# Kernel tuning notes

Measured on AMD Instinct MI355X. Metric: run time of the kernel, lower is better.

Reference implementation:

```python
import jax, jax.numpy as jnp
import numpy as np

B = 8192
D = 1024
NUM_HEADS = 16
HEAD_DIM = D // NUM_HEADS  # 64; only used as the softmax scale


def setup_inputs() -> dict:
    key = jax.random.key(0)
    ks = jax.random.split(key, 7)
    s = 1.0 / np.sqrt(D)
    return {
        "x": jax.random.normal(ks[0], (B, D), dtype=jnp.float32),
        "Wq": jax.random.normal(ks[1], (D, D), dtype=jnp.float32) * s,
        "bq": jax.random.normal(ks[2], (D,), dtype=jnp.float32) * s,
        "Wk": jax.random.normal(ks[3], (D, D), dtype=jnp.float32) * s,
        "bk": jax.random.normal(ks[4], (D,), dtype=jnp.float32) * s,
        "Wv": jax.random.normal(ks[5], (D, D), dtype=jnp.float32) * s,
        "bv": jax.random.normal(ks[6], (D,), dtype=jnp.float32) * s,
    }


def reference(x, Wq, bq, Wk, bk, Wv, bv):
    # Faithful to the torch module: x is 2D [B, D]; attention is over the batch axis.
    # nn.Linear computes x @ W.T + b
    Q = x @ Wq.T + bq            # [B, D]
    K = x @ Wk.T + bk            # [B, D]
    V = x @ Wv.T + bv            # [B, D]
    scale = 1.0 / jnp.sqrt(jnp.float32(HEAD_DIM))
    energy = (Q @ K.T) * scale   # [B, B]
    attn = jax.nn.softmax(energy, axis=-1)
    out = attn @ V               # [B, D]
    # torch: x.permute(0,1).contiguous().view(B, seq_len, -1) -> [B, D, 1]
    return out.reshape(B, D, 1)
```

## Files before the change

kernel.cpp:

```cpp
#include <hip/hip_runtime.h>
#include <hip/hip_bf16.h>

typedef _Float16 half_t;
typedef _Float16 f16x8 __attribute__((ext_vector_type(8)));
typedef _Float16 f16x4 __attribute__((ext_vector_type(4)));
typedef float f32x4 __attribute__((ext_vector_type(4)));
typedef float f32x16 __attribute__((ext_vector_type(16)));

#define B_ROWS 8192
#define D_DIM  1024

__device__ __forceinline__ void gload_lds16(const void* g, void* l)
{
    __builtin_amdgcn_global_load_lds((const __attribute__((address_space(1))) void*)g,
                                     (__attribute__((address_space(3))) void*)l, 16, 0, 0);
}

__global__ __launch_bounds__(256)
void cvt_f32_f16(const float* __restrict__ in, half_t* __restrict__ out, int n)
{
    int i = (blockIdx.x * 256 + threadIdx.x) * 4;
    int stride = gridDim.x * 256 * 4;
    for (; i < n; i += stride) {
        float4 v = *(const float4*)&in[i];
        f16x4 o;
        o[0] = (half_t)v.x; o[1] = (half_t)v.y; o[2] = (half_t)v.z; o[3] = (half_t)v.w;
        *(f16x4*)&out[i] = o;
    }
}

__global__ __launch_bounds__(256)
void transpose_h(const half_t* __restrict__ in, half_t* __restrict__ out, int R, int C)
{
    __shared__ half_t t[64][65];
    int tilesC = C >> 6;
    int bc = blockIdx.x % tilesC;
    int br = blockIdx.x / tilesC;
    int r0 = br * 64, c0 = bc * 64;
    for (int e = threadIdx.x; e < 64 * 64; e += 256) {
        int r = e >> 6, c = e & 63;
        t[r][c] = in[(size_t)(r0 + r) * C + (c0 + c)];
    }
    __syncthreads();
    for (int e = threadIdx.x; e < 64 * 64; e += 256) {
        int r = e >> 6, c = e & 63;
        out[(size_t)(c0 + r) * R + (r0 + c)] = t[c][r];
    }
}

template<int EPI>
__device__ __forceinline__ void gemm8_core(
    const half_t* __restrict__ A, const half_t* __restrict__ Bm,
    const float* __restrict__ aux, float* __restrict__ aux2, int zcol,
    void* __restrict__ Out,
    int lda, int ldb, int ldc, float scale,
    int row0, int col0, int ktile0, int nkt)
{
    __shared__ __align__(16) half_t smem[8 * 8192];
    half_t* As = smem;
    half_t* Bs = smem + 4 * 8192;

    const int tid  = threadIdx.x;
    const int lane = tid & 63;
    const int wid  = tid >> 6;
    const int wr   = wid >> 2;
    const int wcn  = wid & 3;
    const int l31  = lane & 31;
    const int l32  = lane >> 5;

    const int trow  = tid >> 3;
    const int tslot = (tid & 7) ^ (trow & 7);
    const char* Apan[2] = { (const char*)(A + (size_t)row0 * lda),
                            (const char*)(A + (size_t)(row0 + 128) * lda) };
    const char* Bpan[2] = { (const char*)(Bm + (size_t)col0 * ldb),
                            (const char*)(Bm + (size_t)(col0 + 128) * ldb) };
    const size_t aoff[2] = { (size_t)trow * lda * 2 + (size_t)tslot * 16,
                             (size_t)(trow + 64) * lda * 2 + (size_t)tslot * 16 };
    const size_t boff[2] = { (size_t)trow * ldb * 2 + (size_t)tslot * 16,
                             (size_t)(trow + 64) * ldb * 2 + (size_t)tslot * 16 };
    const int dstb[2] = { tid * 16, 8192 + tid * 16 };

    auto stageA = [&](int h, int s, int buf) {
        char* d = (char*)(As + (buf * 2 + h) * 8192);
        const char* g = Apan[h] + (size_t)(ktile0 + s) * 128;
        gload_lds16(g + aoff[0], d + dstb[0]);
        gload_lds16(g + aoff[1], d + dstb[1]);
    };
    auto stageB = [&](int h, int s, int buf) {
        char* d = (char*)(Bs + (buf * 2 + h) * 8192);
        const char* g = Bpan[h] + (size_t)(ktile0 + s) * 128;
        gload_lds16(g + boff[0], d + dstb[0]);
        gload_lds16(g + boff[1], d + dstb[1]);
    };
    auto rdA = [&](int mm, int kc, const half_t* base) -> f16x8 {
        int rih  = wr * 64 + mm * 32 + l31;
        int byte = rih * 128 + (((kc * 2 + l32) ^ (rih & 7)) << 4);
        return *(const f16x8*)((const char*)base + byte);
    };
    auto rdB = [&](int kc, const half_t* base) -> f16x8 {
        int rih  = wcn * 32 + l31;
        int byte = rih * 128 + (((kc * 2 + l32) ^ (rih & 7)) << 4);
        return *(const f16x8*)((const char*)base + byte);
    };

    f32x16 acc[2][2][2] = {};
    f16x8 af[2][4];
    f16x8 bfP[4], bfQ[4];

    {
        int s1 = (nkt > 1) ? 1 : 0;
        stageA(0, 0, 0); stageB(0, 0, 0); stageA(1, 0, 0); stageB(1, 0, 0);
        stageA(0, s1, 1); stageB(0, s1, 1);
    }
    asm volatile("s_waitcnt vmcnt(4)" ::: "memory");
    asm volatile("s_barrier" ::: "memory");

    for (int t = 0; t < nkt; ++t) {
        const int buf = t & 1;
        const half_t* A0 = As + (buf * 2 + 0) * 8192;
        const half_t* A1 = As + (buf * 2 + 1) * 8192;
        const half_t* B0 = Bs + (buf * 2 + 0) * 8192;
        const half_t* B1 = Bs + (buf * 2 + 1) * 8192;
        int t1  = t + 1; int t1s = (t1 < nkt) ? t1 : nkt - 1; int b1 = t1 & 1;
        int t2  = t + 2; int t2s = (t2 < nkt) ? t2 : nkt - 1;

        #pragma unroll
        for (int mm = 0; mm < 2; ++mm)
            #pragma unroll
            for (int kc = 0; kc < 4; ++kc) af[mm][kc] = rdA(mm, kc, A0);
        #pragma unroll
        for (int kc = 0; kc < 4; ++kc) bfP[kc] = rdB(kc, B0);
        stageA(1, t1s, b1);
        asm volatile("s_barrier" ::: "memory");
        __builtin_amdgcn_s_setprio(1);
        #pragma unroll
        for (int kc = 0; kc < 4; ++kc)
            #pragma unroll
            for (int mm = 0; mm < 2; ++mm)
                acc[0][mm][0] = __builtin_amdgcn_mfma_f32_32x32x16_f16(af[mm][kc], bfP[kc], acc[0][mm][0], 0, 0, 0);
        __builtin_amdgcn_s_setprio(0);
        asm volatile("s_barrier" ::: "memory");

        #pragma unroll
        for (int kc = 0; kc < 4; ++kc) bfQ[kc] = rdB(kc, B1);
        stageB(1, t1s, b1);
        asm volatile("s_barrier" ::: "memory");
        __builtin_amdgcn_s_setprio(1);
        #pragma unroll
        for (int kc = 0; kc < 4; ++kc)
            #pragma unroll
            for (int mm = 0; mm < 2; ++mm)
                acc[0][mm][1] = __builtin_amdgcn_mfma_f32_32x32x16_f16(af[mm][kc], bfQ[kc], acc[0][mm][1], 0, 0, 0);
        __builtin_amdgcn_s_setprio(0);
        asm volatile("s_barrier" ::: "memory");

        #pragma unroll
        for (int mm = 0; mm < 2; ++mm)
            #pragma unroll
            for (int kc = 0; kc < 4; ++kc) af[mm][kc] = rdA(mm, kc, A1);
        stageA(0, t2s, buf);
        asm volatile("s_barrier" ::: "memory");
        __builtin_amdgcn_s_setprio(1);
        #pragma unroll
        for (int kc = 0; kc < 4; ++kc)
            #pragma unroll
            for (int mm = 0; mm < 2; ++mm)
                acc[1][mm][0] = __builtin_amdgcn_mfma_f32_32x32x16_f16(af[mm][kc], bfP[kc], acc[1][mm][0], 0, 0, 0);
        __builtin_amdgcn_s_setprio(0);
        asm volatile("s_barrier" ::: "memory");

        stageB(0, t2s, buf);
        asm volatile("s_barrier" ::: "memory");
        __builtin_amdgcn_s_setprio(1);
        #pragma unroll
        for (int kc = 0; kc < 4; ++kc)
            #pragma unroll
            for (int mm = 0; mm < 2; ++mm)
                acc[1][mm][1] = __builtin_amdgcn_mfma_f32_32x32x16_f16(af[mm][kc], bfQ[kc], acc[1][mm][1], 0, 0, 0);
        __builtin_amdgcn_s_setprio(0);
        asm volatile("s_waitcnt vmcnt(4)" ::: "memory");
        asm volatile("s_barrier" ::: "memory");
    }

    if (EPI == 3) {
        asm volatile("s_waitcnt vmcnt(0)" ::: "memory");
        asm volatile("s_barrier" ::: "memory");
        half_t* scratch = smem;
        const int contrib = wcn * 32 + l31;
        #pragma unroll
        for (int h = 0; h < 2; ++h) {
            #pragma unroll
            for (int mm = 0; mm < 2; ++mm) {
                int rl0 = h * 128 + wr * 64 + mm * 32 + 4 * l32;
                #pragma unroll
                for (int g = 0; g < 16; ++g) {
                    int rl = rl0 + (g & 3) + 8 * (g >> 2);
                    float rs = 0.0f;
                    #pragma unroll
                    for (int nh = 0; nh < 2; ++nh) {
                        int gcol = col0 + nh * 128 + wcn * 32 + l31;
                        float e = __expf(acc[h][mm][nh][g] * scale - 20.0f);
                        rs += e;
                        ((half_t*)Out)[(size_t)(row0 + rl) * ldc + gcol] = (half_t)e;
                    }
                    scratch[rl * 136 + contrib] = (half_t)rs;
                }
            }
        }
        asm volatile("s_waitcnt lgkmcnt(0)" ::: "memory");
        asm volatile("s_barrier" ::: "memory");
        {
            int row  = tid >> 1;
            int half = tid & 1;
            const half_t* src = scratch + row * 136 + half * 64;
            float s = 0.0f;
            #pragma unroll
            for (int j = 0; j < 8; ++j) {
                f16x8 v = *(const f16x8*)&src[j * 8];
                #pragma unroll
                for (int tt = 0; tt < 8; ++tt) s += (float)v[tt];
            }
            s += __shfl_xor(s, 1);
            if (half == 0) aux2[(size_t)zcol * B_ROWS + row0 + row] = s;
        }
    } else {
        #pragma unroll
        for (int h = 0; h < 2; ++h) {
            #pragma unroll
            for (int mm = 0; mm < 2; ++mm) {
                int r0 = row0 + h * 128 + wr * 64 + mm * 32 + 4 * l32;
                #pragma unroll
                for (int nh = 0; nh < 2; ++nh) {
                    int gcol = col0 + nh * 128 + wcn * 32 + l31;
                    float badd = (EPI == 0) ? aux[gcol] : 0.0f;
                    #pragma unroll
                    for (int g = 0; g < 16; ++g) {
                        int row = r0 + (g & 3) + 8 * (g >> 2);
                        float v = acc[h][mm][nh][g] * scale + badd;
                        size_t idx = (size_t)row * ldc + gcol;
                        if (EPI == 4)      ((float*)Out)[idx] = v * aux[row];
                        else               ((half_t*)Out)[idx] = (half_t)v;
                    }
                }
            }
        }
    }
}

template<int EPI, int REMAP>
__global__ __launch_bounds__(512, 2)
void gemm8(const half_t* __restrict__ A, const half_t* __restrict__ Bm,
           const float* __restrict__ aux, float* __restrict__ aux2,
           void* __restrict__ Out,
           int lda, int ldb, int ldc, float scale, int nkt)
{
    int bx, by;
    if (REMAP) {
        int L = blockIdx.y * gridDim.x + blockIdx.x;
        int s = L >> 8;
        int u = L & 255;
        int xcd  = u & 7;
        int slot = u >> 3;
        by = (s >> 1) * 16 + xcd * 2 + (slot >> 4);
        bx = (s & 1) * 16 + (slot & 15);
    } else {
        int nwg = gridDim.x * gridDim.y;
        int bid = blockIdx.y * gridDim.x + blockIdx.x;
        if ((nwg & 7) == 0) { int c = nwg >> 3; bid = (bid & 7) * c + (bid >> 3); }
        bx = bid % gridDim.x; by = bid / gridDim.x;
    }
    gemm8_core<EPI>(A, Bm, aux, aux2, bx, Out, lda, ldb, ldc, scale,
                    by * 256, bx * 256, 0, nkt);
}

__global__ __launch_bounds__(512, 2)
void gemm8_qkv(const half_t* __restrict__ xh,
               const half_t* __restrict__ Wq, const half_t* __restrict__ Wk, const half_t* __restrict__ Wv,
               const float* __restrict__ bq, const float* __restrict__ bk, const float* __restrict__ bv,
               half_t* __restrict__ Q, half_t* __restrict__ K, half_t* __restrict__ V)
{
    int z = blockIdx.z;
    const half_t* W = (z == 0) ? Wq : (z == 1) ? Wk : Wv;
    const float*  b = (z == 0) ? bq : (z == 1) ? bk : bv;
    half_t*       O = (z == 0) ? Q  : (z == 1) ? K  : V;
    gemm8_core<0>(xh, W, b, nullptr, 0, O, D_DIM, D_DIM, D_DIM, 1.0f,
                  blockIdx.y * 256, blockIdx.x * 256, 0, D_DIM / 64);
}

__global__ __launch_bounds__(512, 2)
void gemm8_pv(const half_t* __restrict__ E, const half_t* __restrict__ Vt,
              const float* __restrict__ Zinv,
              float* __restrict__ part0, float* __restrict__ part1)
{
    int z = blockIdx.z;
    float* O = z ? part1 : part0;
    gemm8_core<4>(E, Vt, Zinv, nullptr, 0, O, B_ROWS, B_ROWS, D_DIM, 1.0f,
                  blockIdx.y * 256, blockIdx.x * 256, z * (B_ROWS / 128), B_ROWS / 128);
}

__global__ __launch_bounds__(256)
void zreduce(const float* __restrict__ Zpart, float* __restrict__ Zinv, int nrow)
{
    int r = blockIdx.x * 256 + threadIdx.x;
    float s = 0.0f;
    #pragma unroll
    for (int c = 0; c < 32; ++c) s += Zpart[(size_t)c * nrow + r];
    Zinv[r] = 1.0f / s;
}

__global__ __launch_bounds__(256)
void add_f32(const float* __restrict__ a, float* __restrict__ out, int n)
{
    int i = (blockIdx.x * 256 + threadIdx.x) * 4;
    int stride = gridDim.x * 256 * 4;
    for (; i < n; i += stride) {
        float4 x = *(const float4*)&out[i];
        float4 y = *(const float4*)&a[i];
        x.x += y.x; x.y += y.y; x.z += y.z; x.w += y.w;
        *(float4*)&out[i] = x;
    }
}

extern "C" void kernel_launch(void* const* d_in, const int* in_sizes, int n_in,
                              void* d_out, int out_size, void* d_ws, size_t ws_size,
                              hipStream_t stream)
{
    const float* x  = (const float*)d_in[0];
    const float* Wq = (const float*)d_in[1];
    const float* bq = (const float*)d_in[2];
    const float* Wk = (const float*)d_in[3];
    const float* bk = (const float*)d_in[4];
    const float* Wv = (const float*)d_in[5];
    const float* bv = (const float*)d_in[6];
    float* out = (float*)d_out;

    const int Bb = B_ROWS, Dd = D_DIM;

    char* w = (char*)d_ws;
    size_t off = 0;
    auto carve = [&](size_t bytes) {
        void* p = w + off;
        off += (bytes + 255) & ~(size_t)255;
        return p;
    };
    half_t* xh  = (half_t*)carve((size_t)Bb * Dd * 2);
    half_t* Wqh = (half_t*)carve((size_t)Dd * Dd * 2);
    half_t* Wkh = (half_t*)carve((size_t)Dd * Dd * 2);
    half_t* Wvh = (half_t*)carve((size_t)Dd * Dd * 2);
    half_t* Qh  = (half_t*)carve((size_t)Bb * Dd * 2);
    half_t* Kh  = (half_t*)carve((size_t)Bb * Dd * 2);
    half_t* Vh  = (half_t*)carve((size_t)Bb * Dd * 2);
    half_t* S   = (half_t*)carve((size_t)Bb * Bb * 2);
    float*  Zp  = (float*)carve((size_t)32 * Bb * 4);
    float*  Z   = (float*)carve((size_t)Bb * 4);
    half_t* Vt  = xh;
    float*  part1 = (float*)Qh;

    cvt_f32_f16<<<2048, 256, 0, stream>>>(x,  xh,  Bb * Dd);
    cvt_f32_f16<<<1024, 256, 0, stream>>>(Wq, Wqh, Dd * Dd);
    cvt_f32_f16<<<1024, 256, 0, stream>>>(Wk, Wkh, Dd * Dd);
    cvt_f32_f16<<<1024, 256, 0, stream>>>(Wv, Wvh, Dd * Dd);

    dim3 gqkv(Dd / 256, Bb / 256, 3);
    gemm8_qkv<<<gqkv, 512, 0, stream>>>(xh, Wqh, Wkh, Wvh, bq, bk, bv, Qh, Kh, Vh);

    transpose_h<<<(Dd / 64) * (Bb / 64), 256, 0, stream>>>(Vh, Vt, Bb, Dd);

    dim3 gs(Bb / 256, Bb / 256);
    gemm8<3, 1><<<gs, 512, 0, stream>>>(Qh, Kh, nullptr, Zp, S, Dd, Dd, Bb, 0.125f, Dd / 64);

    zreduce<<<Bb / 256, 256, 0, stream>>>(Zp, Z, Bb);

    dim3 gpv(Dd / 256, Bb / 256, 2);
    gemm8_pv<<<gpv, 512, 0, stream>>>(S, Vt, Z, out, part1);
    add_f32<<<2048, 256, 0, stream>>>(part1, out, Bb * Dd);
}
```

Measured before the change: 416.0 us.

## Fuse V transpose into projection GEMM epilogue and merge conversion kernels

Adds a GEMM epilogue that writes the V projection directly in transposed layout, removing the separate transpose kernel and its extra read/write of V. The four fp32-to-fp16 conversion launches are merged into one kernel. The QKV GEMM is split into a QK launch and a separate V launch, which reduces parallelism per launch, and the transposed stores are strided and may coalesce poorly.

After: 410.5 us. Within noise of the previous version (-1.3%).

```diff
diff --git a/kernel.cpp b/kernel.cpp
--- a/kernel.cpp
+++ b/kernel.cpp
@@ -17,34 +17,26 @@
 }
 
 __global__ __launch_bounds__(256)
-void cvt_f32_f16(const float* __restrict__ in, half_t* __restrict__ out, int n)
-{
+void cvt_all(const float* __restrict__ x,  const float* __restrict__ Wq,
+             const float* __restrict__ Wk, const float* __restrict__ Wv,
+             half_t* __restrict__ xh,  half_t* __restrict__ Wqh,
+             half_t* __restrict__ Wkh, half_t* __restrict__ Wvh)
+{
+    const int NX = B_ROWS * D_DIM;
+    const int NW = D_DIM * D_DIM;
+    const int total = NX + 3 * NW;
     int i = (blockIdx.x * 256 + threadIdx.x) * 4;
     int stride = gridDim.x * 256 * 4;
-    for (; i < n; i += stride) {
-        float4 v = *(const float4*)&in[i];
+    for (; i < total; i += stride) {
+        const float* in; half_t* out; int j;
+        if (i < NX)               { in = x;  out = xh;  j = i; }
+        else if (i < NX + NW)     { in = Wq; out = Wqh; j = i - NX; }
+        else if (i < NX + 2 * NW) { in = Wk; out = Wkh; j = i - NX - NW; }
+        else                      { in = Wv; out = Wvh; j = i - NX - 2 * NW; }
+        float4 v = *(const float4*)&in[j];
         f16x4 o;
         o[0] = (half_t)v.x; o[1] = (half_t)v.y; o[2] = (half_t)v.z; o[3] = (half_t)v.w;
-        *(f16x4*)&out[i] = o;
-    }
-}
-
-__global__ __launch_bounds__(256)
-void transpose_h(const half_t* __restrict__ in, half_t* __restrict__ out, int R, int C)
-{
-    __shared__ half_t t[64][65];
-    int tilesC = C >> 6;
-    int bc = blockIdx.x % tilesC;
-    int br = blockIdx.x / tilesC;
-    int r0 = br * 64, c0 = bc * 64;
-    for (int e = threadIdx.x; e < 64 * 64; e += 256) {
-        int r = e >> 6, c = e & 63;
-        t[r][c] = in[(size_t)(r0 + r) * C + (c0 + c)];
-    }
-    __syncthreads();
-    for (int e = threadIdx.x; e < 64 * 64; e += 256) {
-        int r = e >> 6, c = e & 63;
-        out[(size_t)(c0 + r) * R + (r0 + c)] = t[c][r];
+        *(f16x4*)&out[j] = o;
     }
 }
 
@@ -223,6 +215,27 @@
             s += __shfl_xor(s, 1);
             if (half == 0) aux2[(size_t)zcol * B_ROWS + row0 + row] = s;
         }
+    } else if (EPI == 5) {
+        #pragma unroll
+        for (int h = 0; h < 2; ++h) {
+            #pragma unroll
+            for (int mm = 0; mm < 2; ++mm) {
+                int r0 = row0 + h * 128 + wr * 64 + mm * 32 + 4 * l32;
+                #pragma unroll
+                for (int nh = 0; nh < 2; ++nh) {
+                    int gcol = col0 + nh * 128 + wcn * 32 + l31;
+                    float badd = aux[gcol];
+                    #pragma unroll
+                    for (int q = 0; q < 4; ++q) {
+                        f16x4 v4;
+                        #pragma unroll
+                        for (int j = 0; j < 4; ++j)
+                            v4[j] = (half_t)(acc[h][mm][nh][4 * q + j] * scale + badd);
+                        *(f16x4*)&((half_t*)Out)[(size_t)gcol * ldc + r0 + 8 * q] = v4;
+                    }
+                }
+            }
+        }
     } else {
         #pragma unroll
         for (int h = 0; h < 2; ++h) {
@@ -274,16 +287,24 @@
 }
 
 __global__ __launch_bounds__(512, 2)
-void gemm8_qkv(const half_t* __restrict__ xh,
-               const half_t* __restrict__ Wq, const half_t* __restrict__ Wk, const half_t* __restrict__ Wv,
-               const float* __restrict__ bq, const float* __restrict__ bk, const float* __restrict__ bv,
-               half_t* __restrict__ Q, half_t* __restrict__ K, half_t* __restrict__ V)
+void gemm8_qk(const half_t* __restrict__ xh,
+              const half_t* __restrict__ Wq, const half_t* __restrict__ Wk,
+              const float* __restrict__ bq, const float* __restrict__ bk,
+              half_t* __restrict__ Q, half_t* __restrict__ K)
 {
     int z = blockIdx.z;
-    const half_t* W = (z == 0) ? Wq : (z == 1) ? Wk : Wv;
-    const float*  b = (z == 0) ? bq : (z == 1) ? bk : bv;
-    half_t*       O = (z == 0) ? Q  : (z == 1) ? K  : V;
+    const half_t* W = z ? Wk : Wq;
+    const float*  b = z ? bk : bq;
+    half_t*       O = z ? K  : Q;
     gemm8_core<0>(xh, W, b, nullptr, 0, O, D_DIM, D_DIM, D_DIM, 1.0f,
+                  blockIdx.y * 256, blockIdx.x * 256, 0, D_DIM / 64);
+}
+
+__global__ __launch_bounds__(512, 2)
+void gemm8_v(const half_t* __restrict__ xh, const half_t* __restrict__ Wv,
+             const float* __restrict__ bv, half_t* __restrict__ Vt)
+{
+    gemm8_core<5>(xh, Wv, bv, nullptr, 0, Vt, D_DIM, D_DIM, B_ROWS, 1.0f,
                   blockIdx.y * 256, blockIdx.x * 256, 0, D_DIM / 64);
 }
 
@@ -349,22 +370,18 @@
     half_t* Wvh = (half_t*)carve((size_t)Dd * Dd * 2);
     half_t* Qh  = (half_t*)carve((size_t)Bb * Dd * 2);
     half_t* Kh  = (half_t*)carve((size_t)Bb * Dd * 2);
-    half_t* Vh  = (half_t*)carve((size_t)Bb * Dd * 2);
+    half_t* Vt  = (half_t*)carve((size_t)Bb * Dd * 2);
     half_t* S   = (half_t*)carve((size_t)Bb * Bb * 2);
     float*  Zp  = (float*)carve((size_t)32 * Bb * 4);
     float*  Z   = (float*)carve((size_t)Bb * 4);
-    half_t* Vt  = xh;
     float*  part1 = (float*)Qh;
 
-    cvt_f32_f16<<<2048, 256, 0, stream>>>(x,  xh,  Bb * Dd);
-    cvt_f32_f16<<<1024, 256, 0, stream>>>(Wq, Wqh, Dd * Dd);
-    cvt_f32_f16<<<1024, 256, 0, stream>>>(Wk, Wkh, Dd * Dd);
-    cvt_f32_f16<<<1024, 256, 0, stream>>>(Wv, Wvh, Dd * Dd);
-
-    dim3 gqkv(Dd / 256, Bb / 256, 3);
-    gemm8_qkv<<<gqkv, 512, 0, stream>>>(xh, Wqh, Wkh, Wvh, bq, bk, bv, Qh, Kh, Vh);
-
-    transpose_h<<<(Dd / 64) * (Bb / 64), 256, 0, stream>>>(Vh, Vt, Bb, Dd);
+    cvt_all<<<2048, 256, 0, stream>>>(x, Wq, Wk, Wv, xh, Wqh, Wkh, Wvh);
+
+    dim3 gqk(Dd / 256, Bb / 256, 2);
+    gemm8_qk<<<gqk, 512, 0, stream>>>(xh, Wqh, Wkh, bq, bk, Qh, Kh);
+    dim3 gv(Dd / 256, Bb / 256);
+    gemm8_v<<<gv, 512, 0, stream>>>(xh, Wvh, bv, Vt);
 
     dim3 gs(Bb / 256, Bb / 256);
     gemm8<3, 1><<<gs, 512, 0, stream>>>(Qh, Kh, nullptr, Zp, S, Dd, Dd, Bb, 0.125f, Dd / 64);
```
